# Kernel tuning notes

Hardware: AMD Instinct MI355X
Metric: run time of the kernel (lower is better)

## Reference

```python
import jax, jax.numpy as jnp
import numpy as np

HIDDEN = 1024
NUM_HEADS = 16
HEAD_DIM = HIDDEN // NUM_HEADS


def setup_inputs() -> dict:
    key = jax.random.key(0)
    ks = jax.random.split(key, 5)
    scale = 1.0 / np.sqrt(HIDDEN)
    x = jax.random.normal(ks[0], (2, 2048, HIDDEN), dtype=jnp.float32)
    qkv_w = jax.random.uniform(ks[1], (3 * HIDDEN, HIDDEN), jnp.float32, -scale, scale)
    qkv_b = jax.random.uniform(ks[2], (3 * HIDDEN,), jnp.float32, -scale, scale)
    out_w = jax.random.uniform(ks[3], (HIDDEN, HIDDEN), jnp.float32, -scale, scale)
    out_b = jax.random.uniform(ks[4], (HIDDEN,), jnp.float32, -scale, scale)
    return {"x": x, "qkv_w": qkv_w, "qkv_b": qkv_b, "out_w": out_w, "out_b": out_b}


def reference(x, qkv_w, qkv_b, out_w, out_b):
    B, S, _ = x.shape
    qkv = jnp.einsum('bsd,ed->bse', x, qkv_w) + qkv_b  # [B,S,3H]
    q, k, v = jnp.split(qkv, 3, axis=-1)
    # [B,S,H] -> [B,nh,S,hd]
    def to_heads(t):
        return t.reshape(B, S, NUM_HEADS, HEAD_DIM).transpose(0, 2, 1, 3)
    q, k, v = to_heads(q), to_heads(k), to_heads(v)
    scores = jnp.einsum('bhqd,bhkd->bhqk', q, k) / np.sqrt(HEAD_DIM).astype(np.float32)
    attn = jax.nn.softmax(scores, axis=-1)
    o = jnp.einsum('bhqk,bhkd->bhqd', attn, v)
    o = o.transpose(0, 2, 1, 3).reshape(B, S, HIDDEN)
    return jnp.einsum('bsd,ed->bse', o, out_w) + out_b
```

## Files before the change

kernel.cpp:

```cpp
#include <hip/hip_runtime.h>
#include <stdint.h>

typedef __bf16 bf16x8 __attribute__((ext_vector_type(8)));
typedef float  f32x4  __attribute__((ext_vector_type(4)));
typedef float  f32x16 __attribute__((ext_vector_type(16)));
typedef unsigned short u16;
typedef unsigned int   u32;

#define B_  2
#define S_  2048
#define H_  1024
#define NH_ 16
#define HD_ 64
#define QSCL 0.18033688011112042f

__device__ __forceinline__ u16 f2bf(float f) {
  u32 u = __builtin_bit_cast(u32, f);
  return (u16)((u + 0x7FFFu + ((u >> 16) & 1u)) >> 16);
}
__device__ __forceinline__ float ex2(float x) { return __builtin_amdgcn_exp2f(x); }
__device__ __forceinline__ u32 cvtpk(float lo, float hi) {
  u32 r; asm("v_cvt_pk_bf16_f32 %0, %1, %2" : "=v"(r) : "v"(lo), "v"(hi)); return r;
}
__device__ __forceinline__ void gload_lds16(const u16* g, u16* lds) {
  __builtin_amdgcn_global_load_lds(
      (__attribute__((address_space(1))) void*)(void*)g,
      (__attribute__((address_space(3))) void*)lds, 16, 0, 0);
}

__global__ void cvt_all(const float* __restrict__ a, const float* __restrict__ b,
                        const float* __restrict__ c, u16* __restrict__ oa,
                        u16* __restrict__ ob, u16* __restrict__ oc) {
  int i = blockIdx.x * 256 + threadIdx.x;
  const float4* src; ushort4* dst; int j;
  if (i < 1048576)      { src = (const float4*)a; dst = (ushort4*)oa; j = i; }
  else if (i < 1835008) { src = (const float4*)b; dst = (ushort4*)ob; j = i - 1048576; }
  else                  { src = (const float4*)c; dst = (ushort4*)oc; j = i - 1835008; }
  const float4 v = src[j];
  ushort4 o;
  o.x = f2bf(v.x); o.y = f2bf(v.y); o.z = f2bf(v.z); o.w = f2bf(v.w);
  dst[j] = o;
}

__global__ __launch_bounds__(256, 2)
void gemm_qkv(const u16* __restrict__ A, const u16* __restrict__ W,
              const float* __restrict__ bias,
              u16* __restrict__ qb, u16* __restrict__ kb, u16* __restrict__ vb,
              int M, int N, int K)
{
  __shared__ __align__(16) u16 As[2][128 * 32];
  __shared__ __align__(16) u16 Bs[2][128 * 32];
  const int tid = threadIdx.x;
  const int w = tid >> 6, l = tid & 63;
  const int lg = l >> 4, lr = l & 15;
  const int wr = w >> 1, wc = w & 1;
  const int tM = blockIdx.y * 128, tN = blockIdx.x * 128;

  f32x4 acc[4][4];
  const f32x4 z4 = {0.f, 0.f, 0.f, 0.f};
#pragma unroll
  for (int m = 0; m < 4; ++m)
#pragma unroll
    for (int n = 0; n < 4; ++n) acc[m][n] = z4;

  auto STG = [&](int buf, int k0) {
#pragma unroll
    for (int i = 0; i < 2; ++i) {
      const int ch = i * 256 + tid;
      const int row = ch >> 2, cc = (ch & 3) * 8;
      gload_lds16(A + (size_t)(tM + row) * K + k0 + cc, As[buf] + (size_t)(i * 256 + w * 64) * 8);
      gload_lds16(W + (size_t)(tN + row) * K + k0 + cc, Bs[buf] + (size_t)(i * 256 + w * 64) * 8);
    }
  };

  STG(0, 0);
  __syncthreads();

  for (int it = 0; it < K / 32; ++it) {
    const int cur = it & 1;
    if (it + 1 < K / 32) STG(cur ^ 1, (it + 1) * 32);
    bf16x8 af[4], bw[4];
#pragma unroll
    for (int m = 0; m < 4; ++m)
      af[m] = *(const bf16x8*)&As[cur][(wr * 64 + m * 16 + lr) * 32 + lg * 8];
#pragma unroll
    for (int n = 0; n < 4; ++n)
      bw[n] = *(const bf16x8*)&Bs[cur][(wc * 64 + n * 16 + lr) * 32 + lg * 8];
#pragma unroll
    for (int m = 0; m < 4; ++m)
#pragma unroll
      for (int n = 0; n < 4; ++n)
        acc[m][n] = __builtin_amdgcn_mfma_f32_16x16x32_bf16(af[m], bw[n], acc[m][n], 0, 0, 0);
    __syncthreads();
  }

#pragma unroll
  for (int n = 0; n < 4; ++n) {
    const int col = tN + wc * 64 + n * 16 + lr;
    const float bv = bias[col];
    const int t3 = col >> 10, rem = col & 1023;
    const int hh = rem >> 6, dd = rem & 63;
    const float sc = (t3 == 0) ? QSCL : 1.f;
    u16* dst = (t3 == 0) ? qb : (t3 == 1) ? kb : vb;
#pragma unroll
    for (int m = 0; m < 4; ++m)
#pragma unroll
      for (int r = 0; r < 4; ++r) {
        const int row = tM + wr * 64 + m * 16 + lg * 4 + r;
        const int bb = row >> 11, ss = row & 2047;
        dst[((size_t)(bb * NH_ + hh) * S_ + ss) * HD_ + dd] = f2bf((acc[m][n][r] + bv) * sc);
      }
  }
}

__global__ __launch_bounds__(256, 4)
void vtrans(const u16* __restrict__ vb, u16* __restrict__ vtb)
{
  __shared__ u16 Ls[64 * 65];
  const int t = threadIdx.x;
  const int bh = blockIdx.y;
  const int s0 = blockIdx.x * 64;
  const u16* src = vb + ((size_t)bh * S_ + s0) * HD_;
  const int d = t & 63, sy = t >> 6;
#pragma unroll
  for (int p = 0; p < 16; ++p) {
    const int s = p * 4 + sy;
    Ls[s * 65 + d] = src[(size_t)s * HD_ + d];
  }
  __syncthreads();
  const int s = t & 63, dy = t >> 6;
  u16* dst = vtb + (size_t)bh * HD_ * S_ + s0;
#pragma unroll
  for (int p = 0; p < 16; ++p) {
    const int dd = p * 4 + dy;
    dst[(size_t)dd * S_ + s] = Ls[s * 65 + dd];
  }
}

__global__ __launch_bounds__(256, 2)
void gemm_out(const u16* __restrict__ A, const u16* __restrict__ W,
              const float* __restrict__ bias, float* __restrict__ outf,
              int M, int N, int K)
{
  __shared__ __align__(16) u16 As[2][128 * 32];
  __shared__ __align__(16) u16 Bs[2][64 * 32];
  const int tid = threadIdx.x;
  const int w = tid >> 6, l = tid & 63;
  const int lg = l >> 4, lr = l & 15;
  const int tM = blockIdx.y * 128, tN = blockIdx.x * 64;

  f32x4 acc[2][4];
  const f32x4 z4 = {0.f, 0.f, 0.f, 0.f};
#pragma unroll
  for (int m = 0; m < 2; ++m)
#pragma unroll
    for (int n = 0; n < 4; ++n) acc[m][n] = z4;

  auto STG = [&](int buf, int k0) {
#pragma unroll
    for (int i = 0; i < 2; ++i) {
      const int ch = i * 256 + tid;
      const int row = ch >> 2, cc = (ch & 3) * 8;
      gload_lds16(A + (size_t)(tM + row) * K + k0 + cc, As[buf] + (size_t)(i * 256 + w * 64) * 8);
    }
    gload_lds16(W + (size_t)(tN + (tid >> 2)) * K + k0 + (tid & 3) * 8, Bs[buf] + (size_t)(w * 64) * 8);
  };

  STG(0, 0);
  __syncthreads();

  for (int it = 0; it < K / 32; ++it) {
    const int cur = it & 1;
    if (it + 1 < K / 32) STG(cur ^ 1, (it + 1) * 32);
    bf16x8 af[2], bw[4];
#pragma unroll
    for (int m = 0; m < 2; ++m)
      af[m] = *(const bf16x8*)&As[cur][(w * 32 + m * 16 + lr) * 32 + lg * 8];
#pragma unroll
    for (int n = 0; n < 4; ++n)
      bw[n] = *(const bf16x8*)&Bs[cur][(n * 16 + lr) * 32 + lg * 8];
#pragma unroll
    for (int m = 0; m < 2; ++m)
#pragma unroll
      for (int n = 0; n < 4; ++n)
        acc[m][n] = __builtin_amdgcn_mfma_f32_16x16x32_bf16(af[m], bw[n], acc[m][n], 0, 0, 0);
    __syncthreads();
  }

#pragma unroll
  for (int n = 0; n < 4; ++n) {
    const int col = tN + n * 16 + lr;
    const float bv = bias[col];
#pragma unroll
    for (int m = 0; m < 2; ++m)
#pragma unroll
      for (int r = 0; r < 4; ++r) {
        const int row = tM + w * 32 + m * 16 + lg * 4 + r;
        outf[(size_t)row * N + col] = acc[m][n][r] + bv;
      }
  }
}

__global__ __launch_bounds__(256, 2)
void attn_fwd(const u16* __restrict__ qb, const u16* __restrict__ kb,
              const u16* __restrict__ vtb, u16* __restrict__ ob)
{
  __shared__ __align__(16) u16 Kl[2][64 * 64];
  __shared__ __align__(16) u16 Vl[2][64 * 64];

  const int tid = threadIdx.x;
  const int w = tid >> 6, l = tid & 63;
  const int q32 = l & 31, hi = l >> 5;
  const int idx = blockIdx.x;
  const int bh = idx & 31, qt = idx >> 5;
  const int bb = bh >> 4, hh = bh & 15;
  const int q0 = qt * 128 + w * 32;

  bf16x8 qf[4];
#pragma unroll
  for (int ks = 0; ks < 4; ++ks)
    qf[ks] = *(const bf16x8*)&qb[((size_t)bh * S_ + q0 + q32) * HD_ + ks * 16 + hi * 8];

  const f32x16 z16 = {};
  f32x16 acc[2] = {z16, z16};
  float lrun = 0.f;

  const int srow = l >> 3;
  const int scol = ((l & 7) ^ srow) << 3;
  const u16* kbase = kb  + ((size_t)bh * S_  + w * 16 + srow) * HD_ + scol;
  const u16* vbase = vtb + ((size_t)bh * HD_ + w * 16 + srow) * S_  + scol;

  auto STAGE = [&](int buf, int t) {
#pragma unroll
    for (int j = 0; j < 2; ++j) {
      gload_lds16(kbase + (size_t)t * 64 * HD_ + j * 8 * HD_, &Kl[buf][(w * 16 + j * 8) * 64]);
      gload_lds16(vbase + (size_t)t * 64 + j * 8 * S_,        &Vl[buf][(w * 16 + j * 8) * 64]);
    }
  };

  STAGE(0, 0);
  __syncthreads();

  const int sw = q32 & 7;

  for (int t = 0; t < 32; ++t) {
    const int cur = t & 1;
    if (t + 1 < 32) STAGE(cur ^ 1, t + 1);

    f32x16 st[2] = {z16, z16};
    __builtin_amdgcn_s_setprio(1);
#pragma unroll
    for (int kt = 0; kt < 2; ++kt)
#pragma unroll
      for (int ks = 0; ks < 4; ++ks) {
        const bf16x8 kf = *(const bf16x8*)&Kl[cur][(kt * 32 + q32) * 64 + ((((ks << 1) | hi) ^ sw) << 3)];
        st[kt] = __builtin_amdgcn_mfma_f32_32x32x16_bf16(kf, qf[ks], st[kt], 0, 0, 0);
      }
    __builtin_amdgcn_s_setprio(0);

    bf16x8 pa[4];
#pragma unroll
    for (int kt = 0; kt < 2; ++kt) {
      float p[16];
#pragma unroll
      for (int r = 0; r < 16; ++r) p[r] = ex2(st[kt][r]);
#pragma unroll
      for (int g = 0; g < 4; ++g)
        lrun += (p[4 * g] + p[4 * g + 1]) + (p[4 * g + 2] + p[4 * g + 3]);
      u32 wk0[4], wk1[4];
#pragma unroll
      for (int g = 0; g < 4; ++g) {
        wk0[g] = cvtpk(p[4 * g], p[4 * g + 1]);
        wk1[g] = cvtpk(p[4 * g + 2], p[4 * g + 3]);
      }
#pragma unroll
      for (int k2 = 0; k2 < 2; ++k2) {
        u32 a0 = wk0[2 * k2], b0 = wk0[2 * k2 + 1];
        u32 a1 = wk1[2 * k2], b1 = wk1[2 * k2 + 1];
        asm volatile("v_permlane32_swap_b32 %0, %1" : "+v"(a0), "+v"(b0));
        asm volatile("v_permlane32_swap_b32 %0, %1" : "+v"(a1), "+v"(b1));
        uint4 wv = {a0, a1, b0, b1};
        pa[kt * 2 + k2] = __builtin_bit_cast(bf16x8, wv);
      }
    }

    __builtin_amdgcn_s_setprio(1);
#pragma unroll
    for (int dt = 0; dt < 2; ++dt)
#pragma unroll
      for (int ks = 0; ks < 4; ++ks) {
        const bf16x8 vf = *(const bf16x8*)&Vl[cur][(dt * 32 + q32) * 64 + ((((ks << 1) | hi) ^ sw) << 3)];
        acc[dt] = __builtin_amdgcn_mfma_f32_32x32x16_bf16(vf, pa[ks], acc[dt], 0, 0, 0);
      }
    __builtin_amdgcn_s_setprio(0);

    __syncthreads();
  }

  lrun += __shfl_xor(lrun, 32);
  const float linv = 1.f / lrun;
  const size_t orow = ((size_t)(bb * S_ + q0 + q32)) * H_ + hh * HD_;
#pragma unroll
  for (int dt = 0; dt < 2; ++dt)
#pragma unroll
    for (int g = 0; g < 4; ++g) {
      const u32 o0 = cvtpk(acc[dt][4 * g] * linv, acc[dt][4 * g + 1] * linv);
      const u32 o1 = cvtpk(acc[dt][4 * g + 2] * linv, acc[dt][4 * g + 3] * linv);
      uint2 ov; ov.x = o0; ov.y = o1;
      *(uint2*)&ob[orow + dt * 32 + g * 8 + hi * 4] = ov;
    }
}

extern "C" void kernel_launch(void* const* d_in, const int* in_sizes, int n_in,
                              void* d_out, int out_size, void* d_ws, size_t ws_size,
                              hipStream_t stream) {
  const float* x     = (const float*)d_in[0];
  const float* qkv_w = (const float*)d_in[1];
  const float* qkv_b = (const float*)d_in[2];
  const float* out_w = (const float*)d_in[3];
  const float* out_b = (const float*)d_in[4];

  char* ws = (char*)d_ws;
  u16* xb    = (u16*)(ws);
  u16* wqkvb = (u16*)(ws + 8388608);
  u16* wob   = (u16*)(ws + 14680064);
  u16* qb    = (u16*)(ws + 16777216);
  u16* kb    = (u16*)(ws + 25165824);
  u16* vb    = (u16*)(ws + 33554432);
  u16* ob    = (u16*)(ws + 41943040);
  u16* vtb   = xb;

  cvt_all<<<8192, 256, 0, stream>>>(x, qkv_w, out_w, xb, wqkvb, wob);

  gemm_qkv<<<dim3(24, 32), 256, 0, stream>>>(xb, wqkvb, qkv_b,
                                             qb, kb, vb, 4096, 3072, 1024);
  vtrans<<<dim3(32, 32), 256, 0, stream>>>(vb, vtb);
  attn_fwd<<<512, 256, 0, stream>>>(qb, kb, vtb, ob);
  gemm_out<<<dim3(16, 32), 256, 0, stream>>>(ob, wob, out_b, (float*)d_out,
                                             4096, 1024, 1024);
}
```

Baseline: 117.9 us.

## Process two 64-key tiles per iteration in attention loop, halving barriers

The attention inner loop now stages two 64-key K/V sub-tiles per pipeline step (128 keys) and runs 16 iterations instead of 32. All QK^T MFMAs for both sub-tiles are issued back to back, then softmax and PV for each sub-tile follow. This halves the number of __syncthreads and loop iterations and gives the scheduler more independent MFMA work to overlap with exp and conversions. In exchange, LDS usage doubles to 64KB per block, which may limit occupancy at 2 blocks per CU, and register pressure from four score accumulators rises.

```diff
diff --git a/kernel.cpp b/kernel.cpp
--- a/kernel.cpp
+++ b/kernel.cpp
@@ -205,8 +205,8 @@
 void attn_fwd(const u16* __restrict__ qb, const u16* __restrict__ kb,
               const u16* __restrict__ vtb, u16* __restrict__ ob)
 {
-  __shared__ __align__(16) u16 Kl[2][64 * 64];
-  __shared__ __align__(16) u16 Vl[2][64 * 64];
+  __shared__ __align__(16) u16 Kl[2][2][64 * 64];
+  __shared__ __align__(16) u16 Vl[2][2][64 * 64];
 
   const int tid = threadIdx.x;
   const int w = tid >> 6, l = tid & 63;
@@ -232,10 +232,14 @@
 
   auto STAGE = [&](int buf, int t) {
 #pragma unroll
-    for (int j = 0; j < 2; ++j) {
-      gload_lds16(kbase + (size_t)t * 64 * HD_ + j * 8 * HD_, &Kl[buf][(w * 16 + j * 8) * 64]);
-      gload_lds16(vbase + (size_t)t * 64 + j * 8 * S_,        &Vl[buf][(w * 16 + j * 8) * 64]);
-    }
+    for (int s = 0; s < 2; ++s)
+#pragma unroll
+      for (int j = 0; j < 2; ++j) {
+        gload_lds16(kbase + ((size_t)t * 128 + s * 64) * HD_ + j * 8 * HD_,
+                    &Kl[buf][s][(w * 16 + j * 8) * 64]);
+        gload_lds16(vbase + (size_t)t * 128 + s * 64 + j * 8 * S_,
+                    &Vl[buf][s][(w * 16 + j * 8) * 64]);
+      }
   };
 
   STAGE(0, 0);
@@ -243,27 +247,13 @@
 
   const int sw = q32 & 7;
 
-  for (int t = 0; t < 32; ++t) {
-    const int cur = t & 1;
-    if (t + 1 < 32) STAGE(cur ^ 1, t + 1);
-
-    f32x16 st[2] = {z16, z16};
-    __builtin_amdgcn_s_setprio(1);
-#pragma unroll
-    for (int kt = 0; kt < 2; ++kt)
-#pragma unroll
-      for (int ks = 0; ks < 4; ++ks) {
-        const bf16x8 kf = *(const bf16x8*)&Kl[cur][(kt * 32 + q32) * 64 + ((((ks << 1) | hi) ^ sw) << 3)];
-        st[kt] = __builtin_amdgcn_mfma_f32_32x32x16_bf16(kf, qf[ks], st[kt], 0, 0, 0);
-      }
-    __builtin_amdgcn_s_setprio(0);
-
-    bf16x8 pa[4];
+  auto SOFTMAX = [&](f32x16& st0, f32x16& st1, bf16x8* pa) {
 #pragma unroll
     for (int kt = 0; kt < 2; ++kt) {
+      const f32x16& stt = kt ? st1 : st0;
       float p[16];
 #pragma unroll
-      for (int r = 0; r < 16; ++r) p[r] = ex2(st[kt][r]);
+      for (int r = 0; r < 16; ++r) p[r] = ex2(stt[r]);
 #pragma unroll
       for (int g = 0; g < 4; ++g)
         lrun += (p[4 * g] + p[4 * g + 1]) + (p[4 * g + 2] + p[4 * g + 3]);
@@ -283,13 +273,47 @@
         pa[kt * 2 + k2] = __builtin_bit_cast(bf16x8, wv);
       }
     }
-
+  };
+
+  for (int t = 0; t < 16; ++t) {
+    const int cur = t & 1;
+    if (t + 1 < 16) STAGE(cur ^ 1, t + 1);
+
+    f32x16 stA0 = z16, stA1 = z16, stB0 = z16, stB1 = z16;
     __builtin_amdgcn_s_setprio(1);
 #pragma unroll
+    for (int ks = 0; ks < 4; ++ks) {
+      const int so = ((((ks << 1) | hi) ^ sw) << 3);
+      const bf16x8 kfA0 = *(const bf16x8*)&Kl[cur][0][(q32) * 64 + so];
+      const bf16x8 kfA1 = *(const bf16x8*)&Kl[cur][0][(32 + q32) * 64 + so];
+      const bf16x8 kfB0 = *(const bf16x8*)&Kl[cur][1][(q32) * 64 + so];
+      const bf16x8 kfB1 = *(const bf16x8*)&Kl[cur][1][(32 + q32) * 64 + so];
+      stA0 = __builtin_amdgcn_mfma_f32_32x32x16_bf16(kfA0, qf[ks], stA0, 0, 0, 0);
+      stA1 = __builtin_amdgcn_mfma_f32_32x32x16_bf16(kfA1, qf[ks], stA1, 0, 0, 0);
+      stB0 = __builtin_amdgcn_mfma_f32_32x32x16_bf16(kfB0, qf[ks], stB0, 0, 0, 0);
+      stB1 = __builtin_amdgcn_mfma_f32_32x32x16_bf16(kfB1, qf[ks], stB1, 0, 0, 0);
+    }
+    __builtin_amdgcn_s_setprio(0);
+
+    bf16x8 pa[4];
+    SOFTMAX(stA0, stA1, pa);
+    __builtin_amdgcn_s_setprio(1);
+#pragma unroll
     for (int dt = 0; dt < 2; ++dt)
 #pragma unroll
       for (int ks = 0; ks < 4; ++ks) {
-        const bf16x8 vf = *(const bf16x8*)&Vl[cur][(dt * 32 + q32) * 64 + ((((ks << 1) | hi) ^ sw) << 3)];
+        const bf16x8 vf = *(const bf16x8*)&Vl[cur][0][(dt * 32 + q32) * 64 + ((((ks << 1) | hi) ^ sw) << 3)];
+        acc[dt] = __builtin_amdgcn_mfma_f32_32x32x16_bf16(vf, pa[ks], acc[dt], 0, 0, 0);
+      }
+    __builtin_amdgcn_s_setprio(0);
+
+    SOFTMAX(stB0, stB1, pa);
+    __builtin_amdgcn_s_setprio(1);
+#pragma unroll
+    for (int dt = 0; dt < 2; ++dt)
+#pragma unroll
+      for (int ks = 0; ks < 4; ++ks) {
+        const bf16x8 vf = *(const bf16x8*)&Vl[cur][1][(dt * 32 + q32) * 64 + ((((ks << 1) | hi) ^ sw) << 3)];
         acc[dt] = __builtin_amdgcn_mfma_f32_32x32x16_bf16(vf, pa[ks], acc[dt], 0, 0, 0);
       }
     __builtin_amdgcn_s_setprio(0);
```

Measured after the change: 114.9 us. -2.6%, faster.
